# Kernel tuning notes

Measured on AMD Instinct MI355X. Metric: run time of the kernel, lower is better.

## Reference

```python
import jax, jax.numpy as jnp
import numpy as np

NUM_HEADS = 16
N_EMBED = 1024
HEAD_SIZE = 64
BLOCK_SIZE = 2048


def setup_inputs() -> dict:
    key = jax.random.key(0)
    ks = jax.random.split(key, 6)
    B, S, C, H, D = 2, BLOCK_SIZE, N_EMBED, NUM_HEADS, HEAD_SIZE
    x = jax.random.normal(ks[0], (B, S, C), dtype=jnp.float32)
    scale = C ** -0.5
    # per-head q/k/v projections (bias=False), stacked over heads: [H, C, D]
    Wq = jax.random.normal(ks[1], (H, C, D), dtype=jnp.float32) * scale
    Wk = jax.random.normal(ks[2], (H, C, D), dtype=jnp.float32) * scale
    Wv = jax.random.normal(ks[3], (H, C, D), dtype=jnp.float32) * scale
    # output projection Linear(H*D, C)
    Wo = jax.random.normal(ks[4], (H * D, C), dtype=jnp.float32) * ((H * D) ** -0.5)
    bo = jax.random.normal(ks[5], (C,), dtype=jnp.float32) * 0.01
    return {"x": x, "Wq": Wq, "Wk": Wk, "Wv": Wv, "Wo": Wo, "bo": bo}


def reference(x, Wq, Wk, Wv, Wo, bo):
    B, S, C = x.shape
    H, _, D = Wq.shape
    # project: [B, H, S, D]
    q = jnp.einsum("bsc,hcd->bhsd", x, Wq)
    k = jnp.einsum("bsc,hcd->bhsd", x, Wk)
    v = jnp.einsum("bsc,hcd->bhsd", x, Wv)
    # scaled causal attention scores: [B, H, S, S]
    scores = jnp.einsum("bhsd,bhtd->bhst", q, k) * (D ** -0.5)
    causal = jnp.tril(jnp.ones((S, S), dtype=bool))
    scores = jnp.where(causal, scores, jnp.finfo(scores.dtype).min)
    attn = jax.nn.softmax(scores, axis=-1)
    out = jnp.einsum("bhst,bhtd->bhsd", attn, v)  # [B, H, S, D]
    # concat heads -> [B, S, H*D], then output projection
    out = out.transpose(0, 2, 1, 3).reshape(B, S, H * D)
    return out @ Wo + bo
```

## Files before the change

### kernel.cpp

```cpp
#include <hip/hip_runtime.h>
#include <cstdint>
#include <cstddef>

constexpr int SEQ  = 2048;
constexpr int CH   = 1024;
constexpr int NH   = 16;
constexpr int HS   = 64;
constexpr int NB   = 2;
constexpr int HDIM = NH * HS;

typedef __bf16 bf16x8 __attribute__((ext_vector_type(8)));
typedef __bf16 bf16x4 __attribute__((ext_vector_type(4)));
typedef float  f32x4  __attribute__((ext_vector_type(4)));

__device__ __forceinline__ unsigned short f2bf(float f) {
  union { float f; unsigned u; } v; v.f = f;
  unsigned u = v.u;
  u += 0x7fffu + ((u >> 16) & 1u);
  return (unsigned short)(u >> 16);
}
__device__ __forceinline__ float bf2f(unsigned short h) {
  union { unsigned u; float f; } v; v.u = ((unsigned)h) << 16;
  return v.f;
}
__device__ __forceinline__ float load_elem(const void* p, int flag, size_t idx) {
  if (flag) return ((const float*)p)[idx];
  return bf2f(((const unsigned short*)p)[idx]);
}
__device__ __forceinline__ void gl_lds16(const unsigned short* g, unsigned short* l) {
  __builtin_amdgcn_global_load_lds(
      (const __attribute__((address_space(1))) unsigned int*)g,
      (__attribute__((address_space(3))) unsigned int*)l, 16, 0, 0);
}

__device__ int detect_flag_block(const void* p, int n, int tid, int nthr) {
  __shared__ int det_good;
  if (tid == 0) det_good = 0;
  __syncthreads();
  const unsigned short* u = (const unsigned short*)p;
  int good = 0;
  for (int j = tid; j < n; j += nthr) {
    unsigned short v = u[2 * j];
    int e = (v >> 7) & 0xFF;
    if (v != 0 && e >= 90 && e <= 150) good++;
  }
  atomicAdd(&det_good, good);
  __syncthreads();
  return (det_good * 10 >= n * 7) ? 0 : 1;
}

__global__ __launch_bounds__(256) void prep(
    const void* __restrict__ x,  const void* __restrict__ wq,
    const void* __restrict__ wk, const void* __restrict__ wv,
    const void* __restrict__ wo,
    unsigned short* __restrict__ xb,
    unsigned short* __restrict__ wall,
    unsigned short* __restrict__ wot) {
  __shared__ unsigned short tile[32][36];
  int idx = blockIdx.x, tid = threadIdx.x;
  int row = tid >> 3, cg = (tid & 7) * 4;
  int col = tid >> 3, rg = (tid & 7) * 4;
  if (idx < 1024) {
    int f = detect_flag_block(x, 512, tid, 256);
    size_t n4 = (size_t)NB * SEQ * CH / 4;
    for (size_t i = (size_t)idx * 256 + tid; i < n4; i += (size_t)1024 * 256) {
      ushort4 o;
      if (f) {
        float4 v = ((const float4*)x)[i];
        o.x = f2bf(v.x); o.y = f2bf(v.y); o.z = f2bf(v.z); o.w = f2bf(v.w);
      } else {
        o = ((const ushort4*)x)[i];
      }
      ((ushort4*)xb)[i] = o;
    }
  } else if (idx < 4096) {
    int j = idx - 1024;
    int which = j >> 10, hh = (j >> 6) & 15, sub = j & 63;
    const void* src = (which == 0) ? wq : (which == 1) ? wk : wv;
    int f = detect_flag_block(src, 512, tid, 256);
    int c0 = (sub & 1) * 32;
    int r0 = (sub >> 1) * 32;
    size_t boff = (size_t)hh * CH * HS;
    size_t si = boff + (size_t)(r0 + row) * HS + c0 + cg;
    ushort4 t4;
    if (f) {
      float4 v = *(const float4*)((const float*)src + si);
      t4.x = f2bf(v.x); t4.y = f2bf(v.y); t4.z = f2bf(v.z); t4.w = f2bf(v.w);
    } else {
      t4 = *(const ushort4*)((const unsigned short*)src + si);
    }
    *(ushort4*)&tile[row][cg] = t4;
    __syncthreads();
    unsigned short* d = wall + ((size_t)which * NH + hh) * HS * CH;
    ushort4 o;
    o.x = tile[rg + 0][col]; o.y = tile[rg + 1][col];
    o.z = tile[rg + 2][col]; o.w = tile[rg + 3][col];
    *(ushort4*)&d[(size_t)(c0 + col) * CH + r0 + rg] = o;
  } else {
    int sub = idx - 4096;
    int f = detect_flag_block(wo, 512, tid, 256);
    int c0 = (sub & 31) * 32;
    int r0 = (sub >> 5) * 32;
    size_t si = (size_t)(r0 + row) * CH + c0 + cg;
    ushort4 t4;
    if (f) {
      float4 v = *(const float4*)((const float*)wo + si);
      t4.x = f2bf(v.x); t4.y = f2bf(v.y); t4.z = f2bf(v.z); t4.w = f2bf(v.w);
    } else {
      t4 = *(const ushort4*)((const unsigned short*)wo + si);
    }
    *(ushort4*)&tile[row][cg] = t4;
    __syncthreads();
    ushort4 o;
    o.x = tile[rg + 0][col]; o.y = tile[rg + 1][col];
    o.z = tile[rg + 2][col]; o.w = tile[rg + 3][col];
    *(ushort4*)&wot[(size_t)(c0 + col) * HDIM + r0 + rg] = o;
  }
}

__global__ __launch_bounds__(256, 2) void qkv_gemm(
    const unsigned short* __restrict__ xb,
    const unsigned short* __restrict__ wall,
    unsigned short* __restrict__ qo,
    unsigned short* __restrict__ ko,
    unsigned short* __restrict__ vt) {
  __shared__ __attribute__((aligned(16))) unsigned short Al[2][128 * 64];
  __shared__ __attribute__((aligned(16))) unsigned short Bl[2][192 * 64];
  int mt = blockIdx.x, nt = blockIdx.y;
  const unsigned short* A  = xb   + (size_t)mt * 128 * CH;
  const unsigned short* Bm = wall + (size_t)nt * 192 * CH;
  int tid = threadIdx.x, wave = tid >> 6, lane = tid & 63;
  int quad = lane >> 4, l15 = lane & 15;
  int r8 = lane >> 3, c8 = lane & 7;
  int gcol = ((c8 ^ r8) << 3);
  int x7 = l15 & 7;
  int wm = (wave >> 1) * 64, wn = (wave & 1) * 96;
  f32x4 acc[4][6];
  #pragma unroll
  for (int i = 0; i < 4; i++)
    #pragma unroll
    for (int j = 0; j < 6; j++) acc[i][j] = (f32x4){0.f, 0.f, 0.f, 0.f};

  auto stage = [&](int bb, int k0) {
    #pragma unroll
    for (int c = 0; c < 4; c++) {
      int row = wave * 32 + c * 8 + r8;
      gl_lds16(&A[(size_t)row * CH + k0 + gcol], &Al[bb][(wave * 32 + c * 8) * 64]);
    }
    #pragma unroll
    for (int c = 0; c < 6; c++) {
      int row = wave * 48 + c * 8 + r8;
      gl_lds16(&Bm[(size_t)row * CH + k0 + gcol], &Bl[bb][(wave * 48 + c * 8) * 64]);
    }
  };

  stage(0, 0);
  __syncthreads();
  for (int ks = 0; ks < 16; ks++) {
    int bb = ks & 1;
    if (ks < 15) stage(bb ^ 1, (ks + 1) * 64);
    #pragma unroll
    for (int h = 0; h < 2; h++) {
      int cq = ((quad + 4 * h) ^ x7) << 3;
      bf16x8 af[4], bfr[6];
      #pragma unroll
      for (int fm = 0; fm < 4; fm++)
        af[fm] = *reinterpret_cast<const bf16x8*>(&Al[bb][(wm + fm * 16 + l15) * 64 + cq]);
      #pragma unroll
      for (int fn = 0; fn < 6; fn++)
        bfr[fn] = *reinterpret_cast<const bf16x8*>(&Bl[bb][(wn + fn * 16 + l15) * 64 + cq]);
      __builtin_amdgcn_s_setprio(1);
      #pragma unroll
      for (int fm = 0; fm < 4; fm++)
        #pragma unroll
        for (int fn = 0; fn < 6; fn++)
          acc[fm][fn] = __builtin_amdgcn_mfma_f32_16x16x32_bf16(af[fm], bfr[fn], acc[fm][fn], 0, 0, 0);
      __builtin_amdgcn_s_setprio(0);
    }
    __syncthreads();
  }

  #pragma unroll
  for (int fn = 0; fn < 6; fn++) {
    int c0 = nt * 192 + wn + fn * 16;
    int seg = c0 >> 10;
    int hd = (c0 & 1023) + l15;
    int h = hd >> 6, d = hd & 63;
    if (seg < 2) {
      unsigned short* dst = (seg == 0) ? qo : ko;
      float s = (seg == 0) ? 0.18033688011112042f : 1.0f;
      #pragma unroll
      for (int fm = 0; fm < 4; fm++) {
        int m = mt * 128 + wm + fm * 16 + quad * 4;
        int b = m >> 11, s0 = m & 2047;
        #pragma unroll
        for (int r = 0; r < 4; r++)
          dst[(((size_t)b * NH + h) * SEQ + s0 + r) * HS + d] = f2bf(acc[fm][fn][r] * s);
      }
    } else {
      #pragma unroll
      for (int fm = 0; fm < 4; fm++) {
        int m = mt * 128 + wm + fm * 16 + quad * 4;
        int b = m >> 11, s0 = m & 2047;
        ushort4 pk;
        pk.x = f2bf(acc[fm][fn][0]); pk.y = f2bf(acc[fm][fn][1]);
        pk.z = f2bf(acc[fm][fn][2]); pk.w = f2bf(acc[fm][fn][3]);
        *(ushort4*)&vt[(((size_t)b * NH + h) * HS + d) * SEQ + s0] = pk;
      }
    }
  }
}

template <bool MASKED>
__device__ __forceinline__ void soft_pack(const f32x4* s, f32x4& ls,
                                          unsigned short* ptRow, int quad, int tmb) {
  #pragma unroll
  for (int tb = 0; tb < 4; tb++) {
    f32x4 pv;
    #pragma unroll
    for (int r = 0; r < 4; r++) {
      float p = __builtin_amdgcn_exp2f(s[tb][r]);
      if (MASKED) { if (tmb + tb * 16 + quad * 4 + r > 0) p = 0.f; }
      pv[r] = p;
    }
    ls += pv;
    bf16x4 pk;
    pk.x = (__bf16)pv[0]; pk.y = (__bf16)pv[1];
    pk.z = (__bf16)pv[2]; pk.w = (__bf16)pv[3];
    *(bf16x4*)&ptRow[tb * 16 + quad * 4] = pk;
  }
}

template <int QKM, bool PV0, bool PVV>
__device__ __forceinline__ void attn_step(
    const unsigned short (&Kb)[64][64], const unsigned short (&Vp)[64][64],
    unsigned short* p0row, unsigned short* p1row,
    const bf16x8 (&qf)[2][2], f32x4 (&lsum)[2], f32x4 (&accO)[2][4],
    bf16x8 (&bq0)[2], bf16x8 (&bq1)[2],
    int quad, int l15, int tmb) {
  constexpr bool C0 = (QKM <= 1);
  constexpr bool M0 = (QKM == 1);
  constexpr bool M1 = (QKM == 3);
  int x7 = l15 & 7;
  f32x4 s0[4], s1[4];
  #pragma unroll
  for (int tb = 0; tb < 4; tb++) { s0[tb] = (f32x4){0,0,0,0}; s1[tb] = (f32x4){0,0,0,0}; }
  __builtin_amdgcn_s_setprio(1);
  #pragma unroll
  for (int tb = 0; tb < 4; tb++)
    #pragma unroll
    for (int hh = 0; hh < 2; hh++) {
      bf16x8 kf = *reinterpret_cast<const bf16x8*>(
          &Kb[tb * 16 + l15][((hh * 4 + quad) ^ x7) << 3]);
      if (C0) s0[tb] = __builtin_amdgcn_mfma_f32_16x16x32_bf16(kf, qf[0][hh], s0[tb], 0, 0, 0);
      s1[tb] = __builtin_amdgcn_mfma_f32_16x16x32_bf16(kf, qf[1][hh], s1[tb], 0, 0, 0);
    }
  if (PVV) {
    #pragma unroll
    for (int db = 0; db < 4; db++)
      #pragma unroll
      for (int tp = 0; tp < 2; tp++) {
        bf16x8 vf = *reinterpret_cast<const bf16x8*>(
            &Vp[db * 16 + l15][((tp * 4 + quad) ^ x7) << 3]);
        if (PV0) accO[0][db] = __builtin_amdgcn_mfma_f32_16x16x32_bf16(vf, bq0[tp], accO[0][db], 0, 0, 0);
        accO[1][db] = __builtin_amdgcn_mfma_f32_16x16x32_bf16(vf, bq1[tp], accO[1][db], 0, 0, 0);
      }
  }
  __builtin_amdgcn_s_setprio(0);
  if (C0) soft_pack<M0>(s0, lsum[0], p0row, quad, tmb);
  soft_pack<M1>(s1, lsum[1], p1row, quad, tmb);
  #pragma unroll
  for (int tp = 0; tp < 2; tp++) {
    if (C0) bq0[tp] = *reinterpret_cast<const bf16x8*>(&p0row[tp * 32 + quad * 8]);
    bq1[tp] = *reinterpret_cast<const bf16x8*>(&p1row[tp * 32 + quad * 8]);
  }
}

__global__ __launch_bounds__(256) void attn_k(
    const unsigned short* __restrict__ q,
    const unsigned short* __restrict__ k,
    const unsigned short* __restrict__ vt,
    unsigned short* __restrict__ y) {
  __shared__ __attribute__((aligned(16))) unsigned short Kl[3][64][64];
  __shared__ __attribute__((aligned(16))) unsigned short Vl[3][64][64];
  __shared__ __attribute__((aligned(16))) unsigned short Pt[4][16][152];

  int p = blockIdx.x;
  int st0 = p, st1 = 31 - p;
  int bh = blockIdx.y, b = bh >> 4, h = bh & 15;
  const unsigned short* Q0 = q + ((size_t)bh * SEQ + st0 * 64) * HS;
  const unsigned short* Q1 = q + ((size_t)bh * SEQ + st1 * 64) * HS;
  const unsigned short* K  = k  + (size_t)bh * SEQ * HS;
  const unsigned short* V  = vt + (size_t)bh * HS * SEQ;
  int tid = threadIdx.x, wave = tid >> 6, lane = tid & 63;
  int quad = lane >> 4, l15 = lane & 15;
  int lr = tid >> 3, lc = (tid & 7) * 8;
  int sc = (((tid & 7) ^ (lr & 7)) << 3);

  bf16x8 qf[2][2];
  #pragma unroll
  for (int hh = 0; hh < 2; hh++) {
    qf[0][hh] = *reinterpret_cast<const bf16x8*>(
        &Q0[(size_t)(wave * 16 + l15) * HS + hh * 32 + quad * 8]);
    qf[1][hh] = *reinterpret_cast<const bf16x8*>(
        &Q1[(size_t)(wave * 16 + l15) * HS + hh * 32 + quad * 8]);
  }

  f32x4 lsum[2] = {(f32x4){0,0,0,0}, (f32x4){0,0,0,0}};
  f32x4 accO[2][4];
  #pragma unroll
  for (int f = 0; f < 2; f++)
    #pragma unroll
    for (int i = 0; i < 4; i++) accO[f][i] = (f32x4){0.f, 0.f, 0.f, 0.f};
  bf16x8 bq0[2], bq1[2];

  unsigned short* p0row = &Pt[wave][l15][0];
  unsigned short* p1row = &Pt[wave][l15][64];
  int tmb = -(wave * 16 + l15);

  uint4 kr0, kr1, vr0, vr1;
  auto g2r = [&](int kv) {
    kr0 = *(const uint4*)&K[(size_t)(kv * 64 + lr) * HS + lc];
    kr1 = *(const uint4*)&K[(size_t)(kv * 64 + lr + 32) * HS + lc];
    vr0 = *(const uint4*)&V[(size_t)lr * SEQ + kv * 64 + lc];
    vr1 = *(const uint4*)&V[(size_t)(lr + 32) * SEQ + kv * 64 + lc];
  };
  auto r2l = [&](int nb) {
    *(uint4*)&Kl[nb][lr][sc] = kr0; *(uint4*)&Kl[nb][lr + 32][sc] = kr1;
    *(uint4*)&Vl[nb][lr][sc] = vr0; *(uint4*)&Vl[nb][lr + 32][sc] = vr1;
  };

  g2r(0); r2l(0);
  __syncthreads();

  {
    if (st1 > 0) g2r(1);
    if (st0 == 0)
      attn_step<1, false, false>(Kl[0], Vl[2], p0row, p1row, qf, lsum, accO, bq0, bq1, quad, l15, tmb);
    else
      attn_step<0, false, false>(Kl[0], Vl[2], p0row, p1row, qf, lsum, accO, bq0, bq1, quad, l15, tmb);
    if (st1 > 0) r2l(1);
    __syncthreads();
  }
  for (int t = 1; t < st0; t++) {
    g2r(t + 1);
    attn_step<0, true, true>(Kl[t % 3], Vl[(t + 2) % 3], p0row, p1row, qf, lsum, accO, bq0, bq1, quad, l15, tmb);
    r2l((t + 1) % 3);
    __syncthreads();
  }
  if (st0 >= 1) {
    int t = st0;
    g2r(t + 1);
    attn_step<1, true, true>(Kl[t % 3], Vl[(t + 2) % 3], p0row, p1row, qf, lsum, accO, bq0, bq1, quad, l15, tmb);
    r2l((t + 1) % 3);
    __syncthreads();
  }
  {
    int t = st0 + 1;
    bool more = (t < st1);
    if (more) g2r(t + 1);
    if (t == st1)
      attn_step<3, true, true>(Kl[t % 3], Vl[(t + 2) % 3], p0row, p1row, qf, lsum, accO, bq0, bq1, quad, l15, tmb);
    else
      attn_step<2, true, true>(Kl[t % 3], Vl[(t + 2) % 3], p0row, p1row, qf, lsum, accO, bq0, bq1, quad, l15, tmb);
    if (more) r2l((t + 1) % 3);
    __syncthreads();
  }
  for (int t = st0 + 2; t < st1; t++) {
    g2r(t + 1);
    attn_step<2, false, true>(Kl[t % 3], Vl[(t + 2) % 3], p0row, p1row, qf, lsum, accO, bq0, bq1, quad, l15, tmb);
    r2l((t + 1) % 3);
    __syncthreads();
  }
  if (st1 >= st0 + 2) {
    int t = st1;
    attn_step<3, false, true>(Kl[t % 3], Vl[(t + 2) % 3], p0row, p1row, qf, lsum, accO, bq0, bq1, quad, l15, tmb);
  }
  {
    const unsigned short (&Vb)[64][64] = Vl[st1 % 3];
    int x7 = l15 & 7;
    #pragma unroll
    for (int db = 0; db < 4; db++)
      #pragma unroll
      for (int tp = 0; tp < 2; tp++) {
        bf16x8 vf = *reinterpret_cast<const bf16x8*>(
            &Vb[db * 16 + l15][((tp * 4 + quad) ^ x7) << 3]);
        accO[1][db] = __builtin_amdgcn_mfma_f32_16x16x32_bf16(vf, bq1[tp], accO[1][db], 0, 0, 0);
      }
  }

  #pragma unroll
  for (int f = 0; f < 2; f++) {
    float rs = (lsum[f][0] + lsum[f][1]) + (lsum[f][2] + lsum[f][3]);
    rs += __shfl_xor(rs, 16); rs += __shfl_xor(rs, 32);
    float inv = 1.0f / fmaxf(rs, 1e-30f);
    int srow = (f == 0 ? st0 : st1) * 64 + wave * 16 + l15;
    #pragma unroll
    for (int db = 0; db < 4; db++) {
      ushort4 pk;
      pk.x = f2bf(accO[f][db][0] * inv); pk.y = f2bf(accO[f][db][1] * inv);
      pk.z = f2bf(accO[f][db][2] * inv); pk.w = f2bf(accO[f][db][3] * inv);
      *(ushort4*)&y[((size_t)b * SEQ + srow) * HDIM + h * 64 + db * 16 + quad * 4] = pk;
    }
  }
}

__global__ __launch_bounds__(256) void out_gemm(
    const unsigned short* __restrict__ y,
    const unsigned short* __restrict__ wot,
    const void* __restrict__ bo,
    float* __restrict__ out) {
  __shared__ __attribute__((aligned(16))) unsigned short Al[128 * 64];
  __shared__ __attribute__((aligned(16))) unsigned short Bl[64 * 64];
  int tid = threadIdx.x;
  int fbo = detect_flag_block(bo, 512, tid, 256);
  int mt = blockIdx.x, nt = blockIdx.y;
  const unsigned short* A  = y   + (size_t)mt * 128 * HDIM;
  const unsigned short* Bm = wot + (size_t)nt * 64 * HDIM;
  int wave = tid >> 6, lane = tid & 63;
  int quad = lane >> 4, l15 = lane & 15;
  int r8 = lane >> 3, c8 = lane & 7;
  int gcol = ((c8 ^ r8) << 3);
  int x7 = l15 & 7;
  int wm = (wave >> 1) * 64, wn = (wave & 1) * 32;
  f32x4 acc[4][2];
  #pragma unroll
  for (int i = 0; i < 4; i++)
    #pragma unroll
    for (int j = 0; j < 2; j++) acc[i][j] = (f32x4){0.f, 0.f, 0.f, 0.f};

  for (int k0 = 0; k0 < HDIM; k0 += 64) {
    #pragma unroll
    for (int c = 0; c < 4; c++) {
      int row = wave * 32 + c * 8 + r8;
      gl_lds16(&A[(size_t)row * HDIM + k0 + gcol], &Al[(wave * 32 + c * 8) * 64]);
    }
    #pragma unroll
    for (int c = 0; c < 2; c++) {
      int row = wave * 16 + c * 8 + r8;
      gl_lds16(&Bm[(size_t)row * HDIM + k0 + gcol], &Bl[(wave * 16 + c * 8) * 64]);
    }
    __syncthreads();
    #pragma unroll
    for (int h = 0; h < 2; h++) {
      int cq = ((quad + 4 * h) ^ x7) << 3;
      bf16x8 af[4], bfr[2];
      #pragma unroll
      for (int fm = 0; fm < 4; fm++)
        af[fm] = *reinterpret_cast<const bf16x8*>(&Al[(wm + fm * 16 + l15) * 64 + cq]);
      #pragma unroll
      for (int fn = 0; fn < 2; fn++)
        bfr[fn] = *reinterpret_cast<const bf16x8*>(&Bl[(wn + fn * 16 + l15) * 64 + cq]);
      #pragma unroll
      for (int fm = 0; fm < 4; fm++)
        #pragma unroll
        for (int fn = 0; fn < 2; fn++)
          acc[fm][fn] = __builtin_amdgcn_mfma_f32_16x16x32_bf16(af[fm], bfr[fn], acc[fm][fn], 0, 0, 0);
    }
    __syncthreads();
  }

  #pragma unroll
  for (int fn = 0; fn < 2; fn++) {
    int n = nt * 64 + wn + fn * 16 + l15;
    float bias = load_elem(bo, fbo, n);
    #pragma unroll
    for (int fm = 0; fm < 4; fm++) {
      int m = mt * 128 + wm + fm * 16 + quad * 4;
      #pragma unroll
      for (int r = 0; r < 4; r++)
        out[(size_t)(m + r) * CH + n] = acc[fm][fn][r] + bias;
    }
  }
}

extern "C" void kernel_launch(void* const* d_in, const int* in_sizes, int n_in,
                              void* d_out, int out_size, void* d_ws, size_t ws_size,
                              hipStream_t stream) {
  const void* x  = d_in[0];
  const void* Wq = d_in[1];
  const void* Wk = d_in[2];
  const void* Wv = d_in[3];
  const void* Wo = d_in[4];
  const void* bo = d_in[5];
  float* out = (float*)d_out;

  char* ws = (char*)d_ws;
  const size_t MB = 1024 * 1024;
  unsigned short* qb   = (unsigned short*)(ws + 0);
  unsigned short* kb   = (unsigned short*)(ws + 8  * MB);
  unsigned short* vtb  = (unsigned short*)(ws + 16 * MB);
  unsigned short* yb   = (unsigned short*)(ws + 24 * MB);
  unsigned short* wall = (unsigned short*)(ws + 32 * MB);
  unsigned short* wot  = (unsigned short*)(ws + 38 * MB);
  unsigned short* xb   = (unsigned short*)(ws + 40 * MB);

  prep<<<5120, 256, 0, stream>>>(x, Wq, Wk, Wv, Wo, xb, wall, wot);
  qkv_gemm<<<dim3(NB * SEQ / 128, 3 * HDIM / 192), 256, 0, stream>>>(xb, wall, qb, kb, vtb);
  attn_k<<<dim3(16, NB * NH), 256, 0, stream>>>(qb, kb, vtb, yb);
  out_gemm<<<dim3(NB * SEQ / 128, CH / 64), 256, 0, stream>>>(yb, wot, bo, out);
}
```

Measured before the change: 176.5 us.

## Split paired-tile attention blocks into one query tile per block

Each attention block previously handled two query tiles (p and 31-p) to balance causal work, sharing each K/V tile load between them. Now each block handles a single query tile, with the grid doubled to 32x32 and blocks launched longest-first. The K/V shared buffers drop from triple to double buffering, and V fragments are read into registers one step ahead (ping-pong vA/vB) so the delayed PV MFMA no longer needs a third LDS buffer. This raises block count and lowers per-block LDS and register use, but K/V tiles are now loaded from global memory by two blocks instead of one and the per-block work is unbalanced.

```diff
diff --git a/kernel.cpp b/kernel.cpp
--- a/kernel.cpp
+++ b/kernel.cpp
@@ -231,20 +231,23 @@
   }
 }
 
-template <int QKM, bool PV0, bool PVV>
-__device__ __forceinline__ void attn_step(
-    const unsigned short (&Kb)[64][64], const unsigned short (&Vp)[64][64],
-    unsigned short* p0row, unsigned short* p1row,
-    const bf16x8 (&qf)[2][2], f32x4 (&lsum)[2], f32x4 (&accO)[2][4],
-    bf16x8 (&bq0)[2], bf16x8 (&bq1)[2],
+template <bool MASKED, bool DOPV>
+__device__ __forceinline__ void attn_step1(
+    const unsigned short (&Kb)[64][64], const unsigned short (&Vb)[64][64],
+    bf16x8 (&vcur)[8], const bf16x8 (&vprev)[8],
+    unsigned short* prow, const bf16x8 (&qf)[2],
+    f32x4& lsum, f32x4 (&accO)[4], bf16x8 (&bq)[2],
     int quad, int l15, int tmb) {
-  constexpr bool C0 = (QKM <= 1);
-  constexpr bool M0 = (QKM == 1);
-  constexpr bool M1 = (QKM == 3);
   int x7 = l15 & 7;
-  f32x4 s0[4], s1[4];
-  #pragma unroll
-  for (int tb = 0; tb < 4; tb++) { s0[tb] = (f32x4){0,0,0,0}; s1[tb] = (f32x4){0,0,0,0}; }
+  f32x4 s[4];
+  #pragma unroll
+  for (int tb = 0; tb < 4; tb++) s[tb] = (f32x4){0.f, 0.f, 0.f, 0.f};
+  #pragma unroll
+  for (int db = 0; db < 4; db++)
+    #pragma unroll
+    for (int tp = 0; tp < 2; tp++)
+      vcur[db * 2 + tp] = *reinterpret_cast<const bf16x8*>(
+          &Vb[db * 16 + l15][((tp * 4 + quad) ^ x7) << 3]);
   __builtin_amdgcn_s_setprio(1);
   #pragma unroll
   for (int tb = 0; tb < 4; tb++)
@@ -252,28 +255,20 @@
     for (int hh = 0; hh < 2; hh++) {
       bf16x8 kf = *reinterpret_cast<const bf16x8*>(
           &Kb[tb * 16 + l15][((hh * 4 + quad) ^ x7) << 3]);
-      if (C0) s0[tb] = __builtin_amdgcn_mfma_f32_16x16x32_bf16(kf, qf[0][hh], s0[tb], 0, 0, 0);
-      s1[tb] = __builtin_amdgcn_mfma_f32_16x16x32_bf16(kf, qf[1][hh], s1[tb], 0, 0, 0);
-    }
-  if (PVV) {
+      s[tb] = __builtin_amdgcn_mfma_f32_16x16x32_bf16(kf, qf[hh], s[tb], 0, 0, 0);
+    }
+  if (DOPV) {
     #pragma unroll
     for (int db = 0; db < 4; db++)
       #pragma unroll
-      for (int tp = 0; tp < 2; tp++) {
-        bf16x8 vf = *reinterpret_cast<const bf16x8*>(
-            &Vp[db * 16 + l15][((tp * 4 + quad) ^ x7) << 3]);
-        if (PV0) accO[0][db] = __builtin_amdgcn_mfma_f32_16x16x32_bf16(vf, bq0[tp], accO[0][db], 0, 0, 0);
-        accO[1][db] = __builtin_amdgcn_mfma_f32_16x16x32_bf16(vf, bq1[tp], accO[1][db], 0, 0, 0);
-      }
+      for (int tp = 0; tp < 2; tp++)
+        accO[db] = __builtin_amdgcn_mfma_f32_16x16x32_bf16(vprev[db * 2 + tp], bq[tp], accO[db], 0, 0, 0);
   }
   __builtin_amdgcn_s_setprio(0);
-  if (C0) soft_pack<M0>(s0, lsum[0], p0row, quad, tmb);
-  soft_pack<M1>(s1, lsum[1], p1row, quad, tmb);
-  #pragma unroll
-  for (int tp = 0; tp < 2; tp++) {
-    if (C0) bq0[tp] = *reinterpret_cast<const bf16x8*>(&p0row[tp * 32 + quad * 8]);
-    bq1[tp] = *reinterpret_cast<const bf16x8*>(&p1row[tp * 32 + quad * 8]);
-  }
+  soft_pack<MASKED>(s, lsum, prow, quad, tmb);
+  #pragma unroll
+  for (int tp = 0; tp < 2; tp++)
+    bq[tp] = *reinterpret_cast<const bf16x8*>(&prow[tp * 32 + quad * 8]);
 }
 
 __global__ __launch_bounds__(256) void attn_k(
@@ -281,41 +276,34 @@
     const unsigned short* __restrict__ k,
     const unsigned short* __restrict__ vt,
     unsigned short* __restrict__ y) {
-  __shared__ __attribute__((aligned(16))) unsigned short Kl[3][64][64];
-  __shared__ __attribute__((aligned(16))) unsigned short Vl[3][64][64];
-  __shared__ __attribute__((aligned(16))) unsigned short Pt[4][16][152];
-
-  int p = blockIdx.x;
-  int st0 = p, st1 = 31 - p;
+  __shared__ __attribute__((aligned(16))) unsigned short Kl[2][64][64];
+  __shared__ __attribute__((aligned(16))) unsigned short Vl[2][64][64];
+  __shared__ __attribute__((aligned(16))) unsigned short Pt[4][16][88];
+
+  int st = 31 - blockIdx.x;
   int bh = blockIdx.y, b = bh >> 4, h = bh & 15;
-  const unsigned short* Q0 = q + ((size_t)bh * SEQ + st0 * 64) * HS;
-  const unsigned short* Q1 = q + ((size_t)bh * SEQ + st1 * 64) * HS;
-  const unsigned short* K  = k  + (size_t)bh * SEQ * HS;
-  const unsigned short* V  = vt + (size_t)bh * HS * SEQ;
+  const unsigned short* Q = q  + ((size_t)bh * SEQ + st * 64) * HS;
+  const unsigned short* K = k  + (size_t)bh * SEQ * HS;
+  const unsigned short* V = vt + (size_t)bh * HS * SEQ;
   int tid = threadIdx.x, wave = tid >> 6, lane = tid & 63;
   int quad = lane >> 4, l15 = lane & 15;
   int lr = tid >> 3, lc = (tid & 7) * 8;
   int sc = (((tid & 7) ^ (lr & 7)) << 3);
 
-  bf16x8 qf[2][2];
-  #pragma unroll
-  for (int hh = 0; hh < 2; hh++) {
-    qf[0][hh] = *reinterpret_cast<const bf16x8*>(
-        &Q0[(size_t)(wave * 16 + l15) * HS + hh * 32 + quad * 8]);
-    qf[1][hh] = *reinterpret_cast<const bf16x8*>(
-        &Q1[(size_t)(wave * 16 + l15) * HS + hh * 32 + quad * 8]);
-  }
-
-  f32x4 lsum[2] = {(f32x4){0,0,0,0}, (f32x4){0,0,0,0}};
-  f32x4 accO[2][4];
-  #pragma unroll
-  for (int f = 0; f < 2; f++)
-    #pragma unroll
-    for (int i = 0; i < 4; i++) accO[f][i] = (f32x4){0.f, 0.f, 0.f, 0.f};
-  bf16x8 bq0[2], bq1[2];
-
-  unsigned short* p0row = &Pt[wave][l15][0];
-  unsigned short* p1row = &Pt[wave][l15][64];
+  bf16x8 qf[2];
+  #pragma unroll
+  for (int hh = 0; hh < 2; hh++)
+    qf[hh] = *reinterpret_cast<const bf16x8*>(
+        &Q[(size_t)(wave * 16 + l15) * HS + hh * 32 + quad * 8]);
+
+  f32x4 lsum = (f32x4){0.f, 0.f, 0.f, 0.f};
+  f32x4 accO[4];
+  #pragma unroll
+  for (int i = 0; i < 4; i++) accO[i] = (f32x4){0.f, 0.f, 0.f, 0.f};
+  bf16x8 bq[2];
+  bf16x8 vA[8], vB[8];
+
+  unsigned short* prow = &Pt[wave][l15][0];
   int tmb = -(wave * 16 + l15);
 
   uint4 kr0, kr1, vr0, vr1;
@@ -334,74 +322,53 @@
   __syncthreads();
 
   {
-    if (st1 > 0) g2r(1);
-    if (st0 == 0)
-      attn_step<1, false, false>(Kl[0], Vl[2], p0row, p1row, qf, lsum, accO, bq0, bq1, quad, l15, tmb);
+    bool more = (st > 0);
+    if (more) g2r(1);
+    if (st == 0)
+      attn_step1<true,  false>(Kl[0], Vl[0], vA, vB, prow, qf, lsum, accO, bq, quad, l15, tmb);
     else
-      attn_step<0, false, false>(Kl[0], Vl[2], p0row, p1row, qf, lsum, accO, bq0, bq1, quad, l15, tmb);
-    if (st1 > 0) r2l(1);
-    __syncthreads();
-  }
-  for (int t = 1; t < st0; t++) {
+      attn_step1<false, false>(Kl[0], Vl[0], vA, vB, prow, qf, lsum, accO, bq, quad, l15, tmb);
+    if (more) { r2l(1); __syncthreads(); }
+  }
+  for (int t = 1; t < st; t++) {
     g2r(t + 1);
-    attn_step<0, true, true>(Kl[t % 3], Vl[(t + 2) % 3], p0row, p1row, qf, lsum, accO, bq0, bq1, quad, l15, tmb);
-    r2l((t + 1) % 3);
-    __syncthreads();
-  }
-  if (st0 >= 1) {
-    int t = st0;
-    g2r(t + 1);
-    attn_step<1, true, true>(Kl[t % 3], Vl[(t + 2) % 3], p0row, p1row, qf, lsum, accO, bq0, bq1, quad, l15, tmb);
-    r2l((t + 1) % 3);
-    __syncthreads();
-  }
-  {
-    int t = st0 + 1;
-    bool more = (t < st1);
-    if (more) g2r(t + 1);
-    if (t == st1)
-      attn_step<3, true, true>(Kl[t % 3], Vl[(t + 2) % 3], p0row, p1row, qf, lsum, accO, bq0, bq1, quad, l15, tmb);
+    if (t & 1)
+      attn_step1<false, true>(Kl[1], Vl[1], vB, vA, prow, qf, lsum, accO, bq, quad, l15, tmb);
     else
-      attn_step<2, true, true>(Kl[t % 3], Vl[(t + 2) % 3], p0row, p1row, qf, lsum, accO, bq0, bq1, quad, l15, tmb);
-    if (more) r2l((t + 1) % 3);
-    __syncthreads();
-  }
-  for (int t = st0 + 2; t < st1; t++) {
-    g2r(t + 1);
-    attn_step<2, false, true>(Kl[t % 3], Vl[(t + 2) % 3], p0row, p1row, qf, lsum, accO, bq0, bq1, quad, l15, tmb);
-    r2l((t + 1) % 3);
-    __syncthreads();
-  }
-  if (st1 >= st0 + 2) {
-    int t = st1;
-    attn_step<3, false, true>(Kl[t % 3], Vl[(t + 2) % 3], p0row, p1row, qf, lsum, accO, bq0, bq1, quad, l15, tmb);
-  }
-  {
-    const unsigned short (&Vb)[64][64] = Vl[st1 % 3];
-    int x7 = l15 & 7;
+      attn_step1<false, true>(Kl[0], Vl[0], vA, vB, prow, qf, lsum, accO, bq, quad, l15, tmb);
+    r2l((t + 1) & 1);
+    __syncthreads();
+  }
+  if (st >= 1) {
+    if (st & 1)
+      attn_step1<true, true>(Kl[1], Vl[1], vB, vA, prow, qf, lsum, accO, bq, quad, l15, tmb);
+    else
+      attn_step1<true, true>(Kl[0], Vl[0], vA, vB, prow, qf, lsum, accO, bq, quad, l15, tmb);
+  }
+  if (st & 1) {
     #pragma unroll
     for (int db = 0; db < 4; db++)
       #pragma unroll
-      for (int tp = 0; tp < 2; tp++) {
-        bf16x8 vf = *reinterpret_cast<const bf16x8*>(
-            &Vb[db * 16 + l15][((tp * 4 + quad) ^ x7) << 3]);
-        accO[1][db] = __builtin_amdgcn_mfma_f32_16x16x32_bf16(vf, bq1[tp], accO[1][db], 0, 0, 0);
-      }
-  }
-
-  #pragma unroll
-  for (int f = 0; f < 2; f++) {
-    float rs = (lsum[f][0] + lsum[f][1]) + (lsum[f][2] + lsum[f][3]);
-    rs += __shfl_xor(rs, 16); rs += __shfl_xor(rs, 32);
-    float inv = 1.0f / fmaxf(rs, 1e-30f);
-    int srow = (f == 0 ? st0 : st1) * 64 + wave * 16 + l15;
-    #pragma unroll
-    for (int db = 0; db < 4; db++) {
-      ushort4 pk;
-      pk.x = f2bf(accO[f][db][0] * inv); pk.y = f2bf(accO[f][db][1] * inv);
-      pk.z = f2bf(accO[f][db][2] * inv); pk.w = f2bf(accO[f][db][3] * inv);
-      *(ushort4*)&y[((size_t)b * SEQ + srow) * HDIM + h * 64 + db * 16 + quad * 4] = pk;
-    }
+      for (int tp = 0; tp < 2; tp++)
+        accO[db] = __builtin_amdgcn_mfma_f32_16x16x32_bf16(vB[db * 2 + tp], bq[tp], accO[db], 0, 0, 0);
+  } else {
+    #pragma unroll
+    for (int db = 0; db < 4; db++)
+      #pragma unroll
+      for (int tp = 0; tp < 2; tp++)
+        accO[db] = __builtin_amdgcn_mfma_f32_16x16x32_bf16(vA[db * 2 + tp], bq[tp], accO[db], 0, 0, 0);
+  }
+
+  float rs = (lsum[0] + lsum[1]) + (lsum[2] + lsum[3]);
+  rs += __shfl_xor(rs, 16); rs += __shfl_xor(rs, 32);
+  float inv = 1.0f / fmaxf(rs, 1e-30f);
+  int srow = st * 64 + wave * 16 + l15;
+  #pragma unroll
+  for (int db = 0; db < 4; db++) {
+    ushort4 pk;
+    pk.x = f2bf(accO[db][0] * inv); pk.y = f2bf(accO[db][1] * inv);
+    pk.z = f2bf(accO[db][2] * inv); pk.w = f2bf(accO[db][3] * inv);
+    *(ushort4*)&y[((size_t)b * SEQ + srow) * HDIM + h * 64 + db * 16 + quad * 4] = pk;
   }
 }
 
@@ -497,6 +464,6 @@
 
   prep<<<5120, 256, 0, stream>>>(x, Wq, Wk, Wv, Wo, xb, wall, wot);
   qkv_gemm<<<dim3(NB * SEQ / 128, 3 * HDIM / 192), 256, 0, stream>>>(xb, wall, qb, kb, vtb);
-  attn_k<<<dim3(16, NB * NH), 256, 0, stream>>>(qb, kb, vtb, yb);
+  attn_k<<<dim3(32, NB * NH), 256, 0, stream>>>(qb, kb, vtb, yb);
   out_gemm<<<dim3(NB * SEQ / 128, CH / 64), 256, 0, stream>>>(yb, wot, bo, out);
 }
```

Result: slower. 210.3 us (+19.1%).
